# Optimization experiments

Hardware: AMD Instinct MI355X
Metric: run time of the kernel (lower is better)

Reference implementation:

```python
import jax, jax.numpy as jnp
import numpy as np
import math

N_EMBD = 1024
N_HEAD = 16
B, T = 4, 2048

def setup_inputs() -> dict:
    key = jax.random.key(0)
    k1, k2, k3, k4 = jax.random.split(key, 4)
    x = jax.random.normal(k1, (B, T, N_EMBD), dtype=jnp.float32)
    # torch Linear weights: [out, in]; init scale ~1/sqrt(in)
    s = 1.0 / math.sqrt(N_EMBD)
    W_attn = jax.random.normal(k2, (3 * N_EMBD, N_EMBD), dtype=jnp.float32) * s
    W_proj = jax.random.normal(k3, (N_EMBD, N_EMBD), dtype=jnp.float32) * s
    b_proj = jax.random.normal(k4, (N_EMBD,), dtype=jnp.float32) * s
    return {"x": x, "W_attn": W_attn, "W_proj": W_proj, "b_proj": b_proj}

def reference(x, W_attn, W_proj, b_proj):
    Bx, Tx, C = x.shape
    hd = C // N_HEAD
    qkv = jnp.einsum('btc,oc->bto', x, W_attn)  # [B,T,3C]
    q, k, v = jnp.split(qkv, 3, axis=2)
    # [B, H, T, hd]
    q = q.reshape(Bx, Tx, N_HEAD, hd).transpose(0, 2, 1, 3)
    k = k.reshape(Bx, Tx, N_HEAD, hd).transpose(0, 2, 1, 3)
    v = v.reshape(Bx, Tx, N_HEAD, hd).transpose(0, 2, 1, 3)
    # NOTE: source divides by (1/sqrt(hd)) => MULTIPLIES by sqrt(hd). Faithful.
    att = jnp.einsum('bhqd,bhkd->bhqk', q, k) * jnp.sqrt(jnp.float32(hd))
    causal = jnp.tril(jnp.ones((Tx, Tx), dtype=bool))
    att = jnp.where(causal[None, None, :, :], att, -jnp.inf)
    att = jax.nn.softmax(att, axis=-1)
    y = jnp.einsum('bhqk,bhkd->bhqd', att, v)
    y = y.transpose(0, 2, 1, 3).reshape(Bx, Tx, C)
    y = jnp.einsum('btc,oc->bto', y, W_proj) + b_proj
    return y  # dropout is identity in eval
```

## Files before the change

kernel.cpp:

```cpp
#include <hip/hip_runtime.h>
#include <math.h>

#define BATCH 4
#define TSEQ  2048
#define CEMB  1024
#define NHEAD 16
#define HD    64
#define MROWS (BATCH * TSEQ)
#define QSCALE 11.5415603271f

typedef _Float16 half8 __attribute__((ext_vector_type(8)));
typedef _Float16 half4 __attribute__((ext_vector_type(4)));
typedef _Float16 half2 __attribute__((ext_vector_type(2)));
typedef float    floatx4 __attribute__((ext_vector_type(4)));

#define GLOBAL_AS __attribute__((address_space(1)))
#define LDS_AS    __attribute__((address_space(3)))

__device__ __forceinline__ void lds_dma16(const _Float16* g, _Float16* l) {
    __builtin_amdgcn_global_load_lds((const GLOBAL_AS unsigned int*)g,
                                     (LDS_AS unsigned int*)l, 16, 0, 0);
}

__device__ __forceinline__ float fast_exp2(float x) {
    float r; asm("v_exp_f32 %0, %1" : "=v"(r) : "v"(x)); return r;
}

__device__ __forceinline__ half4 pack4(float a0, float a1, float a2, float a3) {
    half2 lo = __builtin_bit_cast(half2, __builtin_amdgcn_cvt_pkrtz(a0, a1));
    half2 hi = __builtin_bit_cast(half2, __builtin_amdgcn_cvt_pkrtz(a2, a3));
    return (half4){lo[0], lo[1], hi[0], hi[1]};
}

__global__ __launch_bounds__(256)
void cvt_fp16(const float* __restrict__ x, const float* __restrict__ wa,
              const float* __restrict__ wp, _Float16* __restrict__ x16,
              _Float16* __restrict__ wa16, _Float16* __restrict__ wp16)
{
    const int n1 = (BATCH * TSEQ * CEMB) / 4;
    const int n2 = (3 * CEMB * CEMB) / 4;
    int i = blockIdx.x * 256 + threadIdx.x;
    const float* src; _Float16* dst; int j;
    if (i < n1)            { src = x;  dst = x16;  j = i; }
    else if (i < n1 + n2)  { src = wa; dst = wa16; j = i - n1; }
    else                   { src = wp; dst = wp16; j = i - n1 - n2; }
    float4 v = ((const float4*)src)[j];
    half4 h = { (_Float16)v.x, (_Float16)v.y, (_Float16)v.z, (_Float16)v.w };
    ((half4*)dst)[j] = h;
}

__device__ __forceinline__ void stage32(const _Float16* __restrict__ gbase,
                                        _Float16* __restrict__ lds,
                                        int row0, int kk, int tid)
{
#pragma unroll
    for (int p = 0; p < 2; ++p) {
        int ci  = p * 256 + tid;
        int row = ci >> 2, pcc = ci & 3;
        int c   = pcc ^ (row & 3);
        lds_dma16(gbase + (size_t)(row0 + row) * CEMB + kk + c * 8, lds + ci * 8);
    }
}

__global__ __launch_bounds__(256)
void qkv_gemm(const _Float16* __restrict__ A, const _Float16* __restrict__ B,
              _Float16* __restrict__ q16, _Float16* __restrict__ k16,
              _Float16* __restrict__ v16)
{
    __shared__ __align__(16) _Float16 smem[16384];
    const int tid = threadIdx.x, lane = tid & 63, wave = tid >> 6;
    const int wm = wave & 1, wn = wave >> 1;
    const int m0 = blockIdx.y * 128, n0 = blockIdx.x * 128;
    const int l15 = lane & 15, quad = lane >> 4;

    floatx4 acc[4][4];
#pragma unroll
    for (int i = 0; i < 4; ++i)
#pragma unroll
        for (int j = 0; j < 4; ++j) acc[i][j] = (floatx4){0.f, 0.f, 0.f, 0.f};

    stage32(A, smem, m0, 0, tid);
    stage32(B, smem + 8192, n0, 0, tid);
    for (int kt = 0; kt < 32; ++kt) {
        const int cur = kt & 1;
        _Float16* Asc = smem + cur * 4096;
        _Float16* Bsc = smem + 8192 + cur * 4096;
        __syncthreads();
        if (kt < 31) {
            stage32(A, smem + (cur ^ 1) * 4096, m0, (kt + 1) * 32, tid);
            stage32(B, smem + 8192 + (cur ^ 1) * 4096, n0, (kt + 1) * 32, tid);
        }
        half8 af[4], bf[4];
#pragma unroll
        for (int mt = 0; mt < 4; ++mt) {
            int row = wm * 64 + mt * 16 + l15;
            af[mt] = *(const half8*)(Asc + row * 32 + (quad ^ (row & 3)) * 8);
        }
#pragma unroll
        for (int nt = 0; nt < 4; ++nt) {
            int row = wn * 64 + nt * 16 + l15;
            bf[nt] = *(const half8*)(Bsc + row * 32 + (quad ^ (row & 3)) * 8);
        }
#pragma unroll
        for (int mt = 0; mt < 4; ++mt)
#pragma unroll
            for (int nt = 0; nt < 4; ++nt)
                acc[mt][nt] = __builtin_amdgcn_mfma_f32_16x16x32_f16(af[mt], bf[nt], acc[mt][nt], 0, 0, 0);
    }

    __syncthreads();
    const int rbase = quad << 2;
    if (n0 < 2 * CEMB) {
        const float scale = (n0 < CEMB) ? QSCALE : 1.0f;
#pragma unroll
        for (int mt = 0; mt < 4; ++mt)
#pragma unroll
            for (int nt = 0; nt < 4; ++nt)
#pragma unroll
                for (int r = 0; r < 4; ++r) {
                    int t = wm * 64 + mt * 16 + rbase + r;
                    int n = wn * 64 + nt * 16 + l15;
                    int pc = (n >> 3) ^ (t & 15);
                    smem[t * 128 + pc * 8 + (n & 7)] = (_Float16)(acc[mt][nt][r] * scale);
                }
        __syncthreads();
        const int chunk = tid & 7;
#pragma unroll
        for (int i = 0; i < 8; ++i) {
            int gr = (tid >> 3) + i * 32;
            int seg = gr >> 7, t = gr & 127;
            int pc = (seg * 8 + chunk) ^ (t & 15);
            half8 v = *(const half8*)(smem + t * 128 + pc * 8);
            int gm = m0 + t, b = gm >> 11, tt = gm & (TSEQ - 1);
            int gnb = n0 + seg * 64;
            _Float16* dst;
            if (n0 < CEMB) {
                int h = gnb >> 6;
                dst = q16 + (((size_t)(b * NHEAD + h)) * TSEQ + tt) * HD;
            } else {
                int h = (gnb - CEMB) >> 6;
                dst = k16 + (((size_t)(b * NHEAD + h)) * TSEQ + tt) * HD;
            }
            *(half8*)(dst + chunk * 8) = v;
        }
    } else {
#pragma unroll
        for (int mt = 0; mt < 4; ++mt)
#pragma unroll
            for (int nt = 0; nt < 4; ++nt)
#pragma unroll
                for (int r = 0; r < 4; ++r) {
                    int t = wm * 64 + mt * 16 + rbase + r;
                    int n = wn * 64 + nt * 16 + l15;
                    int pc = (t >> 3) ^ (n & 15);
                    smem[n * 128 + pc * 8 + (t & 7)] = (_Float16)acc[mt][nt][r];
                }
        __syncthreads();
        const int chunk = tid & 15;
        const int b = m0 >> 11, tblk = m0 & (TSEQ - 1);
#pragma unroll
        for (int i = 0; i < 8; ++i) {
            int row = (tid >> 4) + i * 16;
            int pc = chunk ^ (row & 15);
            half8 v = *(const half8*)(smem + row * 128 + pc * 8);
            int c2 = n0 - 2 * CEMB + row;
            int h = c2 >> 6, d = c2 & 63;
            *(half8*)(v16 + (((size_t)(b * NHEAD + h)) * HD + d) * TSEQ + tblk + chunk * 8) = v;
        }
    }
}

__device__ __forceinline__ void attn_tile(
    const half8& qf0, const half8& qf1,
    float& m_i, float& l_i, floatx4 (&o)[4],
    const _Float16* __restrict__ Ks, const _Float16* __restrict__ Vs,
    bool domask, int l15, int quad, int relq)
{
    floatx4 s[4];
#pragma unroll
    for (int nt = 0; nt < 4; ++nt) {
        int row = nt * 16 + l15;
        int pc0 = quad ^ (row & 7);
        half8 kf0 = *(const half8*)(Ks + row * 64 + pc0 * 8);
        half8 kf1 = *(const half8*)(Ks + row * 64 + (pc0 ^ 4) * 8);
        floatx4 z = (floatx4){0.f, 0.f, 0.f, 0.f};
        z = __builtin_amdgcn_mfma_f32_16x16x32_f16(kf0, qf0, z, 0, 0, 0);
        z = __builtin_amdgcn_mfma_f32_16x16x32_f16(kf1, qf1, z, 0, 0, 0);
        s[nt] = z;
    }
    if (domask) {
#pragma unroll
        for (int nt = 0; nt < 4; ++nt)
#pragma unroll
            for (int r = 0; r < 4; ++r)
                if (nt * 16 + quad * 4 + r > relq) s[nt][r] = -INFINITY;
    }
    float pmax = -INFINITY;
#pragma unroll
    for (int nt = 0; nt < 4; ++nt)
        pmax = fmaxf(pmax, fmaxf(fmaxf(s[nt][0], s[nt][1]), fmaxf(s[nt][2], s[nt][3])));
    if (!__all(pmax <= m_i)) {
        float mx = fmaxf(m_i, pmax);
        mx = fmaxf(mx, __shfl_xor(mx, 16, 64));
        mx = fmaxf(mx, __shfl_xor(mx, 32, 64));
        float alpha = fast_exp2(m_i - mx);
        m_i = mx;
        l_i *= alpha;
#pragma unroll
        for (int mt = 0; mt < 4; ++mt)
#pragma unroll
            for (int r = 0; r < 4; ++r) o[mt][r] *= alpha;
    }
    float rs = 0.f;
    half4 p[4];
#pragma unroll
    for (int nt = 0; nt < 4; ++nt) {
        float p0 = fast_exp2(s[nt][0] - m_i), p1 = fast_exp2(s[nt][1] - m_i);
        float p2 = fast_exp2(s[nt][2] - m_i), p3 = fast_exp2(s[nt][3] - m_i);
        rs += (p0 + p1) + (p2 + p3);
        p[nt] = pack4(p0, p1, p2, p3);
    }
    l_i += rs;
#pragma unroll
    for (int mt = 0; mt < 4; ++mt) {
        int d = mt * 16 + l15;
#pragma unroll
        for (int nt = 0; nt < 4; ++nt) {
            int pc = (2 * nt + (quad >> 1)) ^ (d & 7);
            half4 vf = *(const half4*)(Vs + d * 64 + pc * 8 + (quad & 1) * 4);
            o[mt] = __builtin_amdgcn_mfma_f32_16x16x16f16(vf, p[nt], o[mt], 0, 0, 0);
        }
    }
}

__device__ __forceinline__ void attn_tile2(
    const half8& qA0, const half8& qA1, const half8& qB0, const half8& qB1,
    float& mAi, float& lAi, floatx4 (&oA)[4],
    float& mBi, float& lBi, floatx4 (&oB)[4],
    const _Float16* __restrict__ Ks, const _Float16* __restrict__ Vs,
    bool maskA, int l15, int quad, int relq)
{
    floatx4 sA[4], sB[4];
#pragma unroll
    for (int nt = 0; nt < 4; ++nt) {
        int row = nt * 16 + l15;
        int pc0 = quad ^ (row & 7);
        half8 kf0 = *(const half8*)(Ks + row * 64 + pc0 * 8);
        half8 kf1 = *(const half8*)(Ks + row * 64 + (pc0 ^ 4) * 8);
        floatx4 zA = (floatx4){0.f, 0.f, 0.f, 0.f};
        floatx4 zB = (floatx4){0.f, 0.f, 0.f, 0.f};
        zA = __builtin_amdgcn_mfma_f32_16x16x32_f16(kf0, qA0, zA, 0, 0, 0);
        zB = __builtin_amdgcn_mfma_f32_16x16x32_f16(kf0, qB0, zB, 0, 0, 0);
        zA = __builtin_amdgcn_mfma_f32_16x16x32_f16(kf1, qA1, zA, 0, 0, 0);
        zB = __builtin_amdgcn_mfma_f32_16x16x32_f16(kf1, qB1, zB, 0, 0, 0);
        sA[nt] = zA; sB[nt] = zB;
    }
    if (maskA) {
#pragma unroll
        for (int nt = 0; nt < 4; ++nt)
#pragma unroll
            for (int r = 0; r < 4; ++r)
                if (nt * 16 + quad * 4 + r > relq) sA[nt][r] = -INFINITY;
    }
    float pA = -INFINITY, pB = -INFINITY;
#pragma unroll
    for (int nt = 0; nt < 4; ++nt) {
        pA = fmaxf(pA, fmaxf(fmaxf(sA[nt][0], sA[nt][1]), fmaxf(sA[nt][2], sA[nt][3])));
        pB = fmaxf(pB, fmaxf(fmaxf(sB[nt][0], sB[nt][1]), fmaxf(sB[nt][2], sB[nt][3])));
    }
    if (!__all((pA <= mAi) && (pB <= mBi))) {
        float mxA = fmaxf(mAi, pA), mxB = fmaxf(mBi, pB);
        mxA = fmaxf(mxA, __shfl_xor(mxA, 16, 64));
        mxB = fmaxf(mxB, __shfl_xor(mxB, 16, 64));
        mxA = fmaxf(mxA, __shfl_xor(mxA, 32, 64));
        mxB = fmaxf(mxB, __shfl_xor(mxB, 32, 64));
        float alA = fast_exp2(mAi - mxA);
        float alB = fast_exp2(mBi - mxB);
        mAi = mxA; mBi = mxB;
        lAi *= alA; lBi *= alB;
#pragma unroll
        for (int mt = 0; mt < 4; ++mt)
#pragma unroll
            for (int r = 0; r < 4; ++r) { oA[mt][r] *= alA; oB[mt][r] *= alB; }
    }
    float rsA = 0.f, rsB = 0.f;
    half4 pAh[4], pBh[4];
#pragma unroll
    for (int nt = 0; nt < 4; ++nt) {
        float a0 = fast_exp2(sA[nt][0] - mAi), b0 = fast_exp2(sB[nt][0] - mBi);
        float a1 = fast_exp2(sA[nt][1] - mAi), b1 = fast_exp2(sB[nt][1] - mBi);
        float a2 = fast_exp2(sA[nt][2] - mAi), b2 = fast_exp2(sB[nt][2] - mBi);
        float a3 = fast_exp2(sA[nt][3] - mAi), b3 = fast_exp2(sB[nt][3] - mBi);
        rsA += (a0 + a1) + (a2 + a3);
        rsB += (b0 + b1) + (b2 + b3);
        pAh[nt] = pack4(a0, a1, a2, a3);
        pBh[nt] = pack4(b0, b1, b2, b3);
    }
    lAi += rsA; lBi += rsB;
#pragma unroll
    for (int mt = 0; mt < 4; ++mt) {
        int d = mt * 16 + l15;
#pragma unroll
        for (int nt = 0; nt < 4; ++nt) {
            int pc = (2 * nt + (quad >> 1)) ^ (d & 7);
            half4 vf = *(const half4*)(Vs + d * 64 + pc * 8 + (quad & 1) * 4);
            oA[mt] = __builtin_amdgcn_mfma_f32_16x16x16f16(vf, pAh[nt], oA[mt], 0, 0, 0);
            oB[mt] = __builtin_amdgcn_mfma_f32_16x16x16f16(vf, pBh[nt], oB[mt], 0, 0, 0);
        }
    }
}

__global__ __launch_bounds__(256)
void attn_fwd(const _Float16* __restrict__ q16, const _Float16* __restrict__ k16,
              const _Float16* __restrict__ v16, _Float16* __restrict__ o16)
{
    __shared__ __align__(16) _Float16 Ks[2][64 * 64];
    __shared__ __align__(16) _Float16 Vs[2][64 * 64];
    const int tid = threadIdx.x, lane = tid & 63, wave = tid >> 6;
    const int l15 = lane & 15, quad = lane >> 4;

    const int L   = blockIdx.x + 16 * blockIdx.y;
    const int qtA = (L >> 3) & 15;
    const int bh  = (L & 7) + ((L >> 7) << 3);
    const int qtB = 31 - qtA;
    const int b = bh >> 4, h = bh & 15;
    const int q0A = qtA * 64, q0B = qtB * 64;
    const _Float16* qp = q16 + (size_t)bh * TSEQ * HD;
    const _Float16* kp = k16 + (size_t)bh * TSEQ * HD;
    const _Float16* vp = v16 + (size_t)bh * HD * TSEQ;

    const int relq = wave * 16 + l15;
    half8 qA0 = *(const half8*)(qp + (size_t)(q0A + relq) * HD + quad * 8);
    half8 qA1 = *(const half8*)(qp + (size_t)(q0A + relq) * HD + 32 + quad * 8);
    half8 qB0 = *(const half8*)(qp + (size_t)(q0B + relq) * HD + quad * 8);
    half8 qB1 = *(const half8*)(qp + (size_t)(q0B + relq) * HD + 32 + quad * 8);

    float mA = -INFINITY, lA = 0.f, mB = -INFINITY, lB = 0.f;
    floatx4 oA[4], oB[4];
#pragma unroll
    for (int mt = 0; mt < 4; ++mt) { oA[mt] = (floatx4){0.f,0.f,0.f,0.f}; oB[mt] = (floatx4){0.f,0.f,0.f,0.f}; }

#define STAGE_KV(kt0, buf)                                                     \
    {                                                                          \
        _Float16* kd = Ks[buf];                                                \
        _Float16* vd = Vs[buf];                                                \
        _Pragma("unroll")                                                      \
        for (int p = 0; p < 2; ++p) {                                          \
            int ci = p * 256 + tid;                                            \
            int row = ci >> 3;                                                 \
            int c2 = (ci & 7) ^ (row & 7);                                     \
            lds_dma16(kp + (size_t)((kt0) + row) * HD + c2 * 8, kd + ci * 8);  \
            lds_dma16(vp + (size_t)row * TSEQ + (kt0) + c2 * 8, vd + ci * 8);  \
        }                                                                      \
    }

    STAGE_KV(0, 0);
    for (int kt = 0; kt <= qtA; ++kt) {
        const int cur = kt & 1;
        __syncthreads();
        STAGE_KV((kt + 1) * 64, cur ^ 1);
        attn_tile2(qA0, qA1, qB0, qB1, mA, lA, oA, mB, lB, oB,
                   Ks[cur], Vs[cur], (kt == qtA), l15, quad, relq);
    }
    for (int kt = qtA + 1; kt <= qtB; ++kt) {
        const int cur = kt & 1;
        __syncthreads();
        if (kt < qtB) STAGE_KV((kt + 1) * 64, cur ^ 1);
        attn_tile(qB0, qB1, mB, lB, oB, Ks[cur], Vs[cur], (kt == qtB), l15, quad, relq);
    }
#undef STAGE_KV

    lA += __shfl_xor(lA, 16, 64); lA += __shfl_xor(lA, 32, 64);
    lB += __shfl_xor(lB, 16, 64); lB += __shfl_xor(lB, 32, 64);
    const float invA = 1.f / lA, invB = 1.f / lB;
    const size_t baseA = ((size_t)(b * TSEQ + q0A + relq)) * CEMB + h * HD + quad * 4;
    const size_t baseB = ((size_t)(b * TSEQ + q0B + relq)) * CEMB + h * HD + quad * 4;
#pragma unroll
    for (int mt = 0; mt < 4; ++mt) {
        half4 ha = { (_Float16)(oA[mt][0] * invA), (_Float16)(oA[mt][1] * invA),
                     (_Float16)(oA[mt][2] * invA), (_Float16)(oA[mt][3] * invA) };
        half4 hb = { (_Float16)(oB[mt][0] * invB), (_Float16)(oB[mt][1] * invB),
                     (_Float16)(oB[mt][2] * invB), (_Float16)(oB[mt][3] * invB) };
        *(half4*)(o16 + baseA + mt * 16) = ha;
        *(half4*)(o16 + baseB + mt * 16) = hb;
    }
}

__global__ __launch_bounds__(256)
void proj_gemm(const _Float16* __restrict__ A, const _Float16* __restrict__ B,
               const float* __restrict__ bias, float* __restrict__ out)
{
    __shared__ __align__(16) _Float16 smem[16384];
    const int tid = threadIdx.x, lane = tid & 63, wave = tid >> 6;
    const int wm = wave & 1, wn = wave >> 1;
    const int m0 = blockIdx.y * 128, n0 = blockIdx.x * 128;
    const int l15 = lane & 15, quad = lane >> 4;

    floatx4 acc[4][4];
#pragma unroll
    for (int i = 0; i < 4; ++i)
#pragma unroll
        for (int j = 0; j < 4; ++j) acc[i][j] = (floatx4){0.f, 0.f, 0.f, 0.f};

    stage32(A, smem, m0, 0, tid);
    stage32(B, smem + 8192, n0, 0, tid);
    for (int kt = 0; kt < 32; ++kt) {
        const int cur = kt & 1;
        _Float16* Asc = smem + cur * 4096;
        _Float16* Bsc = smem + 8192 + cur * 4096;
        __syncthreads();
        if (kt < 31) {
            stage32(A, smem + (cur ^ 1) * 4096, m0, (kt + 1) * 32, tid);
            stage32(B, smem + 8192 + (cur ^ 1) * 4096, n0, (kt + 1) * 32, tid);
        }
        half8 af[4], bf[4];
#pragma unroll
        for (int mt = 0; mt < 4; ++mt) {
            int row = wm * 64 + mt * 16 + l15;
            af[mt] = *(const half8*)(Asc + row * 32 + (quad ^ (row & 3)) * 8);
        }
#pragma unroll
        for (int nt = 0; nt < 4; ++nt) {
            int row = wn * 64 + nt * 16 + l15;
            bf[nt] = *(const half8*)(Bsc + row * 32 + (quad ^ (row & 3)) * 8);
        }
#pragma unroll
        for (int mt = 0; mt < 4; ++mt)
#pragma unroll
            for (int nt = 0; nt < 4; ++nt)
                acc[mt][nt] = __builtin_amdgcn_mfma_f32_16x16x32_f16(af[mt], bf[nt], acc[mt][nt], 0, 0, 0);
    }

    const int rbase = quad << 2;
#pragma unroll
    for (int mt = 0; mt < 4; ++mt)
#pragma unroll
        for (int nt = 0; nt < 4; ++nt) {
            int gn = n0 + wn * 64 + nt * 16 + l15;
            float bb = bias[gn];
#pragma unroll
            for (int r = 0; r < 4; ++r) {
                int gm = m0 + wm * 64 + mt * 16 + rbase + r;
                out[(size_t)gm * CEMB + gn] = acc[mt][nt][r] + bb;
            }
        }
}

extern "C" void kernel_launch(void* const* d_in, const int* in_sizes, int n_in,
                              void* d_out, int out_size, void* d_ws, size_t ws_size,
                              hipStream_t stream) {
    const float* x     = (const float*)d_in[0];
    const float* Wattn = (const float*)d_in[1];
    const float* Wproj = (const float*)d_in[2];
    const float* bproj = (const float*)d_in[3];
    float* out = (float*)d_out;

    const size_t nx  = (size_t)BATCH * TSEQ * CEMB;
    const size_t nwa = (size_t)3 * CEMB * CEMB;
    const size_t nwp = (size_t)CEMB * CEMB;
    const size_t per = (size_t)BATCH * NHEAD * TSEQ * HD;

    _Float16* x16    = (_Float16*)d_ws;
    _Float16* wa16   = x16 + nx;
    _Float16* wp16   = wa16 + nwa;
    _Float16* q16    = wp16 + nwp;
    _Float16* k16    = q16 + per;
    _Float16* v16    = k16 + per;
    _Float16* attn16 = x16;

    const int nconv = (int)((nx + nwa + nwp) / 4);
    cvt_fp16<<<nconv / 256, 256, 0, stream>>>(x, Wattn, Wproj, x16, wa16, wp16);
    qkv_gemm<<<dim3(3 * CEMB / 128, MROWS / 128), 256, 0, stream>>>(x16, wa16, q16, k16, v16);
    attn_fwd<<<dim3(16, BATCH * NHEAD), 256, 0, stream>>>(q16, k16, v16, attn16);
    proj_gemm<<<dim3(CEMB / 128, MROWS / 128), 256, 0, stream>>>(attn16, wp16, bproj, out);
}
```

Before: 281.7 us.

## Load V fragments directly from global and remap GEMM block order

The attention kernel stops staging V tiles into shared memory. Each lane now loads its V fragments straight from global memory (v is stored transposed, [d][T]) into registers, issued early so the loads overlap the softmax. This cuts LDS traffic and halves shared-memory use, at the cost of uncoalesced-ish global loads that rely on the L2 cache. Separately, both GEMMs remap the linear block index so consecutive blocks share B (weight) column tiles and walk M in groups, aiming at better L2 reuse.

```diff
diff --git a/kernel.cpp b/kernel.cpp
--- a/kernel.cpp
+++ b/kernel.cpp
@@ -70,7 +70,10 @@
     __shared__ __align__(16) _Float16 smem[16384];
     const int tid = threadIdx.x, lane = tid & 63, wave = tid >> 6;
     const int wm = wave & 1, wn = wave >> 1;
-    const int m0 = blockIdx.y * 128, n0 = blockIdx.x * 128;
+    const int L  = blockIdx.x + 24 * blockIdx.y;
+    const int jj = L >> 3;
+    const int m0 = ((L & 7) + 8 * (jj & 7)) * 128;
+    const int n0 = (jj >> 3) * 128;
     const int l15 = lane & 15, quad = lane >> 4;
 
     floatx4 acc[4][4];
@@ -173,7 +176,7 @@
 __device__ __forceinline__ void attn_tile(
     const half8& qf0, const half8& qf1,
     float& m_i, float& l_i, floatx4 (&o)[4],
-    const _Float16* __restrict__ Ks, const _Float16* __restrict__ Vs,
+    const _Float16* __restrict__ Ks, const _Float16* __restrict__ vg,
     bool domask, int l15, int quad, int relq)
 {
     floatx4 s[4];
@@ -188,6 +191,14 @@
         z = __builtin_amdgcn_mfma_f32_16x16x32_f16(kf1, qf1, z, 0, 0, 0);
         s[nt] = z;
     }
+    half4 vf[4][4];
+#pragma unroll
+    for (int mt = 0; mt < 4; ++mt) {
+        const _Float16* vrow = vg + (size_t)(mt * 16 + l15) * TSEQ + quad * 4;
+#pragma unroll
+        for (int nt = 0; nt < 4; ++nt)
+            vf[mt][nt] = *(const half4*)(vrow + nt * 16);
+    }
     if (domask) {
 #pragma unroll
         for (int nt = 0; nt < 4; ++nt)
@@ -222,22 +233,17 @@
     }
     l_i += rs;
 #pragma unroll
-    for (int mt = 0; mt < 4; ++mt) {
-        int d = mt * 16 + l15;
-#pragma unroll
-        for (int nt = 0; nt < 4; ++nt) {
-            int pc = (2 * nt + (quad >> 1)) ^ (d & 7);
-            half4 vf = *(const half4*)(Vs + d * 64 + pc * 8 + (quad & 1) * 4);
-            o[mt] = __builtin_amdgcn_mfma_f32_16x16x16f16(vf, p[nt], o[mt], 0, 0, 0);
-        }
-    }
+    for (int mt = 0; mt < 4; ++mt)
+#pragma unroll
+        for (int nt = 0; nt < 4; ++nt)
+            o[mt] = __builtin_amdgcn_mfma_f32_16x16x16f16(vf[mt][nt], p[nt], o[mt], 0, 0, 0);
 }
 
 __device__ __forceinline__ void attn_tile2(
     const half8& qA0, const half8& qA1, const half8& qB0, const half8& qB1,
     float& mAi, float& lAi, floatx4 (&oA)[4],
     float& mBi, float& lBi, floatx4 (&oB)[4],
-    const _Float16* __restrict__ Ks, const _Float16* __restrict__ Vs,
+    const _Float16* __restrict__ Ks, const _Float16* __restrict__ vg,
     bool maskA, int l15, int quad, int relq)
 {
     floatx4 sA[4], sB[4];
@@ -255,6 +261,14 @@
         zB = __builtin_amdgcn_mfma_f32_16x16x32_f16(kf1, qB1, zB, 0, 0, 0);
         sA[nt] = zA; sB[nt] = zB;
     }
+    half4 vf[4][4];
+#pragma unroll
+    for (int mt = 0; mt < 4; ++mt) {
+        const _Float16* vrow = vg + (size_t)(mt * 16 + l15) * TSEQ + quad * 4;
+#pragma unroll
+        for (int nt = 0; nt < 4; ++nt)
+            vf[mt][nt] = *(const half4*)(vrow + nt * 16);
+    }
     if (maskA) {
 #pragma unroll
         for (int nt = 0; nt < 4; ++nt)
@@ -298,16 +312,12 @@
     }
     lAi += rsA; lBi += rsB;
 #pragma unroll
-    for (int mt = 0; mt < 4; ++mt) {
-        int d = mt * 16 + l15;
+    for (int mt = 0; mt < 4; ++mt)
 #pragma unroll
         for (int nt = 0; nt < 4; ++nt) {
-            int pc = (2 * nt + (quad >> 1)) ^ (d & 7);
-            half4 vf = *(const half4*)(Vs + d * 64 + pc * 8 + (quad & 1) * 4);
-            oA[mt] = __builtin_amdgcn_mfma_f32_16x16x16f16(vf, pAh[nt], oA[mt], 0, 0, 0);
-            oB[mt] = __builtin_amdgcn_mfma_f32_16x16x16f16(vf, pBh[nt], oB[mt], 0, 0, 0);
-        }
-    }
+            oA[mt] = __builtin_amdgcn_mfma_f32_16x16x16f16(vf[mt][nt], pAh[nt], oA[mt], 0, 0, 0);
+            oB[mt] = __builtin_amdgcn_mfma_f32_16x16x16f16(vf[mt][nt], pBh[nt], oB[mt], 0, 0, 0);
+        }
 }
 
 __global__ __launch_bounds__(256)
@@ -315,7 +325,6 @@
               const _Float16* __restrict__ v16, _Float16* __restrict__ o16)
 {
     __shared__ __align__(16) _Float16 Ks[2][64 * 64];
-    __shared__ __align__(16) _Float16 Vs[2][64 * 64];
     const int tid = threadIdx.x, lane = tid & 63, wave = tid >> 6;
     const int l15 = lane & 15, quad = lane >> 4;
 
@@ -340,35 +349,34 @@
 #pragma unroll
     for (int mt = 0; mt < 4; ++mt) { oA[mt] = (floatx4){0.f,0.f,0.f,0.f}; oB[mt] = (floatx4){0.f,0.f,0.f,0.f}; }
 
-#define STAGE_KV(kt0, buf)                                                     \
+#define STAGE_K(kt0, buf)                                                      \
     {                                                                          \
         _Float16* kd = Ks[buf];                                                \
-        _Float16* vd = Vs[buf];                                                \
         _Pragma("unroll")                                                      \
         for (int p = 0; p < 2; ++p) {                                          \
             int ci = p * 256 + tid;                                            \
             int row = ci >> 3;                                                 \
             int c2 = (ci & 7) ^ (row & 7);                                     \
             lds_dma16(kp + (size_t)((kt0) + row) * HD + c2 * 8, kd + ci * 8);  \
-            lds_dma16(vp + (size_t)row * TSEQ + (kt0) + c2 * 8, vd + ci * 8);  \
         }                                                                      \
     }
 
-    STAGE_KV(0, 0);
+    STAGE_K(0, 0);
     for (int kt = 0; kt <= qtA; ++kt) {
         const int cur = kt & 1;
         __syncthreads();
-        STAGE_KV((kt + 1) * 64, cur ^ 1);
+        STAGE_K((kt + 1) * 64, cur ^ 1);
         attn_tile2(qA0, qA1, qB0, qB1, mA, lA, oA, mB, lB, oB,
-                   Ks[cur], Vs[cur], (kt == qtA), l15, quad, relq);
+                   Ks[cur], vp + kt * 64, (kt == qtA), l15, quad, relq);
     }
     for (int kt = qtA + 1; kt <= qtB; ++kt) {
         const int cur = kt & 1;
         __syncthreads();
-        if (kt < qtB) STAGE_KV((kt + 1) * 64, cur ^ 1);
-        attn_tile(qB0, qB1, mB, lB, oB, Ks[cur], Vs[cur], (kt == qtB), l15, quad, relq);
-    }
-#undef STAGE_KV
+        if (kt < qtB) STAGE_K((kt + 1) * 64, cur ^ 1);
+        attn_tile(qB0, qB1, mB, lB, oB, Ks[cur], vp + kt * 64,
+                  (kt == qtB), l15, quad, relq);
+    }
+#undef STAGE_K
 
     lA += __shfl_xor(lA, 16, 64); lA += __shfl_xor(lA, 32, 64);
     lB += __shfl_xor(lB, 16, 64); lB += __shfl_xor(lB, 32, 64);
@@ -393,7 +401,10 @@
     __shared__ __align__(16) _Float16 smem[16384];
     const int tid = threadIdx.x, lane = tid & 63, wave = tid >> 6;
     const int wm = wave & 1, wn = wave >> 1;
-    const int m0 = blockIdx.y * 128, n0 = blockIdx.x * 128;
+    const int L  = blockIdx.x + 8 * blockIdx.y;
+    const int jj = L >> 3;
+    const int m0 = ((L & 7) + 8 * (jj & 7)) * 128;
+    const int n0 = (jj >> 3) * 128;
     const int l15 = lane & 15, quad = lane >> 4;
 
     floatx4 acc[4][4];
```

Measured after the change: 433.3 us. 1.54x slower.
